# Optimization experiments

Measured on AMD Instinct MI355X. Metric: run time of the kernel, lower is better.

## Reference

```python
import jax, jax.numpy as jnp
import numpy as np


def setup_inputs() -> dict:
    key = jax.random.key(0)
    ks = jax.random.split(key, 9)
    B, L, Dh, Din = 8, 2048, 256, 1024  # Dh = hidden_size = input_dim // num_heads
    s = 0.05
    return {
        "x": jax.random.normal(ks[0], (B, L, Dh), dtype=jnp.float32),
        "Wq": jax.random.normal(ks[1], (Dh, Dh), dtype=jnp.float32) * s,
        "bq": jax.random.normal(ks[2], (Dh,), dtype=jnp.float32) * s,
        "Wk": jax.random.normal(ks[3], (Dh, Dh), dtype=jnp.float32) * s,
        "bk": jax.random.normal(ks[4], (Dh,), dtype=jnp.float32) * s,
        "Wv": jax.random.normal(ks[5], (Dh, Dh), dtype=jnp.float32) * s,
        "bv": jax.random.normal(ks[6], (Dh,), dtype=jnp.float32) * s,
        "Wo": jax.random.normal(ks[7], (Dh, Din), dtype=jnp.float32) * s,
        "bo": jax.random.normal(ks[8], (Din,), dtype=jnp.float32) * s,
        "num_heads": 4,
    }


def reference(x, Wq, bq, Wk, bk, Wv, bv, Wo, bo, num_heads):
    B, L, d = x.shape  # d == hidden_size; scale uses this full dim per the source
    H = num_heads
    hd = d // H
    # QKV projections (weights stored [in, out])
    Q = (x @ Wq + bq).reshape(B, L, H, hd).transpose(0, 2, 1, 3)  # [B,H,L,hd]
    K = (x @ Wk + bk).reshape(B, L, H, hd).transpose(0, 2, 1, 3)
    V = (x @ Wv + bv).reshape(B, L, H, hd).transpose(0, 2, 1, 3)
    scale = 1.0 / jnp.sqrt(jnp.float32(d))  # source divides by dim**0.5 with dim = x.shape[-1]
    scores = jnp.einsum("bhqd,bhkd->bhqk", Q, K) * scale  # [B,H,L,L]
    weights = jax.nn.softmax(scores, axis=-1)
    # dropout is identity in eval mode
    ctx = jnp.einsum("bhqk,bhkd->bhqd", weights, V)  # [B,H,L,hd]
    ctx = ctx.transpose(0, 2, 1, 3).reshape(B, L, d)
    return ctx @ Wo + bo  # [B,L,input_dim]
```

## Files before the change

kernel.cpp:

```cpp
#include <hip/hip_runtime.h>

#define SEQ   2048
#define NH    4
#define HD    64
#define DH    256
#define DIN   1024
#define MTOK  16384
#define BH    32

typedef _Float16 half8 __attribute__((ext_vector_type(8)));
typedef _Float16 half4 __attribute__((ext_vector_type(4)));
typedef float    floatx4 __attribute__((ext_vector_type(4)));

__device__ __forceinline__ floatx4 mfma16(half8 a, half8 b, floatx4 c) {
    return __builtin_amdgcn_mfma_f32_16x16x32_f16(a, b, c, 0, 0, 0);
}

#if __has_builtin(__builtin_amdgcn_exp2f)
#define EXP2(x) __builtin_amdgcn_exp2f(x)
#else
#define EXP2(x) exp2f(x)
#endif

__device__ __forceinline__ int swz(int r, int g) {
    return r * 64 + ((g ^ (r & 7)) << 3);
}

__device__ __forceinline__ void glds16(const _Float16* g, _Float16* l) {
    __builtin_amdgcn_global_load_lds(
        (const __attribute__((address_space(1))) void*)g,
        (__attribute__((address_space(3))) void*)l, 16, 0, 0);
}

#define QSCALE 0.09016844005556021f

__global__ __launch_bounds__(256) void cvt_kernel(
    const float* __restrict__ x, const float* __restrict__ Wq,
    const float* __restrict__ Wk, const float* __restrict__ Wv,
    const float* __restrict__ Wo, _Float16* __restrict__ xh,
    _Float16* __restrict__ Wt)
{
    const int t = threadIdx.x;
    if (blockIdx.x < 2048) {
        const size_t i = ((size_t)blockIdx.x * 256 + t) * 8;
        const float4 f0 = *(const float4*)(x + i);
        const float4 f1 = *(const float4*)(x + i + 4);
        half8 h;
        h[0]=(_Float16)f0.x; h[1]=(_Float16)f0.y; h[2]=(_Float16)f0.z; h[3]=(_Float16)f0.w;
        h[4]=(_Float16)f1.x; h[5]=(_Float16)f1.y; h[6]=(_Float16)f1.z; h[7]=(_Float16)f1.w;
        *(half8*)(xh + i) = h;
        return;
    }
    const int wb = blockIdx.x - 2048;
    const int nb = (wb % 28) * 64;
    const int kb = (wb / 28) * 64;
    const float* src; int ld, nc0;
    if (nb < 768) {
        src = (nb < 256) ? Wq : (nb < 512) ? Wk : Wv;
        ld = DH; nc0 = nb & 255;
    } else { src = Wo; ld = DIN; nc0 = nb - 768; }

    __shared__ float Ts[64][65];
    const int c = t & 63, r0 = t >> 6;
#pragma unroll
    for (int rr = 0; rr < 16; rr++)
        Ts[r0 + rr * 4][c] = src[(size_t)(kb + r0 + rr * 4) * ld + nc0 + c];
    __syncthreads();
    const int nr = t >> 2, kc = (t & 3) * 16;
    _Float16 hv[16];
#pragma unroll
    for (int j = 0; j < 16; j++) hv[j] = (_Float16)Ts[kc + j][nr];
    *(half8*)&Wt[(size_t)(nb + nr) * 256 + kb + kc]     = *(half8*)&hv[0];
    *(half8*)&Wt[(size_t)(nb + nr) * 256 + kb + kc + 8] = *(half8*)&hv[8];
}

__global__ __launch_bounds__(256) void qkv_kernel(
    const _Float16* __restrict__ xh, const _Float16* __restrict__ Wt,
    const float* __restrict__ bq, const float* __restrict__ bk,
    const float* __restrict__ bv,
    _Float16* __restrict__ Qo, _Float16* __restrict__ Ko, _Float16* __restrict__ Vt)
{
    const int mb = blockIdx.x * 128;
    const int nb = blockIdx.y * 128;
    const int t = threadIdx.x, lane = t & 63, w = t >> 6;
    const int quad = lane >> 4, l16 = lane & 15;
    const int wr = (w >> 1) * 64, wc = (w & 1) * 64;

    __shared__ _Float16 Ah[128 * 64];
    __shared__ _Float16 Bh[128 * 64];

    floatx4 acc[4][4] = {};

    const int srow = w * 8 + (lane >> 3);
    const int slg  = (lane & 7) ^ ((lane >> 3) & 7);
    const int sbase = w * 64;

    for (int k0 = 0; k0 < DH; k0 += 64) {
        __syncthreads();
#pragma unroll
        for (int c = 0; c < 4; c++) {
            glds16(xh + (size_t)(mb + c * 32 + srow) * DH + k0 + slg * 8,
                   &Ah[(c * 256 + sbase) * 8]);
            glds16(Wt + (size_t)(nb + c * 32 + srow) * DH + k0 + slg * 8,
                   &Bh[(c * 256 + sbase) * 8]);
        }
        __syncthreads();
#pragma unroll
        for (int kh = 0; kh < 2; kh++) {
            half8 af[4], bf[4];
#pragma unroll
            for (int i = 0; i < 4; i++) {
                af[i] = *(const half8*)&Ah[swz(wr + i * 16 + l16, kh * 4 + quad)];
                bf[i] = *(const half8*)&Bh[swz(wc + i * 16 + l16, kh * 4 + quad)];
            }
#pragma unroll
            for (int mt = 0; mt < 4; mt++)
#pragma unroll
                for (int nt = 0; nt < 4; nt++)
                    acc[mt][nt] = mfma16(af[mt], bf[nt], acc[mt][nt]);
        }
    }

    const int which = nb >> 8;
    const float* bias = (which == 0) ? bq : (which == 1) ? bk : bv;
    const float qs = (which == 0) ? QSCALE : 1.0f;

#pragma unroll
    for (int nt = 0; nt < 4; nt++) {
        const int col = nb + wc + nt * 16 + l16;
        const int c2 = col & 255;
        const float bb = bias[c2];
        const int h = c2 >> 6, hd = c2 & 63;
#pragma unroll
        for (int mt = 0; mt < 4; mt++) {
            const int mr0 = mb + wr + mt * 16 + quad * 4;
            const int b = mr0 >> 11, lt0 = mr0 & (SEQ - 1);
            const int bh = b * NH + h;
            if (which == 2) {
                half4 hv;
#pragma unroll
                for (int i = 0; i < 4; i++) hv[i] = (_Float16)(acc[mt][nt][i] + bb);
                *(half4*)&Vt[((size_t)bh * HD + hd) * SEQ + lt0] = hv;
            } else {
                _Float16* dst = ((which == 0) ? Qo : Ko) + ((size_t)bh * SEQ + lt0) * HD + hd;
#pragma unroll
                for (int i = 0; i < 4; i++)
                    dst[(size_t)i * HD] = (_Float16)((acc[mt][nt][i] + bb) * qs);
            }
        }
    }
}

__global__ __launch_bounds__(256, 4) void attn_kernel(
    const _Float16* __restrict__ Q, const _Float16* __restrict__ K,
    const _Float16* __restrict__ Vt, _Float16* __restrict__ Opart,
    float* __restrict__ Lsum, int kspan)
{
    const int bh = blockIdx.y, qb = blockIdx.x * 128, ks = blockIdx.z;
    const int t = threadIdx.x, lane = t & 63, w = t >> 6;
    const int quad = lane >> 4, l16 = lane & 15;

    __shared__ _Float16 Ksm[64 * 64];
    __shared__ _Float16 Vsm[64 * 64];
    __shared__ _Float16 Psm[4 * 32 * 64];

    const _Float16* Kbh = K + (size_t)bh * SEQ * HD;
    const _Float16* Vbh = Vt + (size_t)bh * HD * SEQ;

    half8 qf[2][2];
#pragma unroll
    for (int qt = 0; qt < 2; qt++) {
        const _Float16* qp = Q + ((size_t)bh * SEQ + qb + w * 32 + qt * 16 + l16) * HD;
        qf[qt][0] = *(const half8*)(qp + quad * 8);
        qf[qt][1] = *(const half8*)(qp + 32 + quad * 8);
    }

    floatx4 oacc[2][4] = {};
    float lsum[2] = {0.f, 0.f};

    const int srow = w * 8 + (lane >> 3);
    const int slg  = (lane & 7) ^ ((lane >> 3) & 7);
    const int sbase = w * 64;
    const int pbase = w * 2048;
    const int kb0 = ks * kspan, kb1 = kb0 + kspan;

    for (int kb = kb0; kb < kb1; kb += 64) {
        __syncthreads();
#pragma unroll
        for (int c = 0; c < 2; c++) {
            glds16(Kbh + (size_t)(kb + c * 32 + srow) * HD + slg * 8,
                   &Ksm[(c * 256 + sbase) * 8]);
            glds16(Vbh + (size_t)(c * 32 + srow) * SEQ + kb + slg * 8,
                   &Vsm[(c * 256 + sbase) * 8]);
        }
        __syncthreads();

#pragma unroll
        for (int kt = 0; kt < 4; kt++) {
            const half8 kf0 = *(const half8*)&Ksm[swz(kt * 16 + l16, quad)];
            const half8 kf1 = *(const half8*)&Ksm[swz(kt * 16 + l16, 4 + quad)];
#pragma unroll
            for (int qt = 0; qt < 2; qt++) {
                floatx4 a = {};
                a = mfma16(kf0, qf[qt][0], a);
                a = mfma16(kf1, qf[qt][1], a);
                const float p0 = EXP2(a[0]), p1 = EXP2(a[1]);
                const float p2 = EXP2(a[2]), p3 = EXP2(a[3]);
                lsum[qt] += (p0 + p1) + (p2 + p3);
                half4 hp;
                hp[0] = (_Float16)p0; hp[1] = (_Float16)p1;
                hp[2] = (_Float16)p2; hp[3] = (_Float16)p3;
                const int g = kt * 2 + (quad >> 1);
                *(half4*)&Psm[pbase + (qt * 16 + l16) * 64 +
                              ((g ^ (l16 & 7)) << 3) + (quad & 1) * 4] = hp;
            }
        }

#pragma unroll
        for (int k2 = 0; k2 < 2; k2++) {
            half8 pf[2];
#pragma unroll
            for (int qt = 0; qt < 2; qt++)
                pf[qt] = *(const half8*)&Psm[pbase + swz(qt * 16 + l16, k2 * 4 + quad)];
#pragma unroll
            for (int nt = 0; nt < 4; nt++) {
                const half8 vf = *(const half8*)&Vsm[swz(nt * 16 + l16, k2 * 4 + quad)];
#pragma unroll
                for (int qt = 0; qt < 2; qt++)
                    oacc[qt][nt] = mfma16(pf[qt], vf, oacc[qt][nt]);
            }
        }
    }

#pragma unroll
    for (int qt = 0; qt < 2; qt++) {
        lsum[qt] += __shfl_xor(lsum[qt], 16, 64);
        lsum[qt] += __shfl_xor(lsum[qt], 32, 64);
        if (quad == 0)
            Lsum[((size_t)(ks * BH + bh)) * SEQ + qb + w * 32 + qt * 16 + l16] = lsum[qt];
    }
    _Float16* op = Opart + (((size_t)(ks * BH + bh)) * SEQ + qb + w * 32) * HD;
#pragma unroll
    for (int qt = 0; qt < 2; qt++)
#pragma unroll
        for (int i = 0; i < 4; i++) {
            const int r = qt * 16 + quad * 4 + i;
#pragma unroll
            for (int nt = 0; nt < 4; nt++)
                op[(size_t)r * HD + nt * 16 + l16] = (_Float16)oacc[qt][nt][i];
        }
}

__global__ __launch_bounds__(256) void reduce_kernel(
    const _Float16* __restrict__ Opart, const float* __restrict__ Lsum,
    _Float16* __restrict__ ctx, int nks)
{
    const size_t i = ((size_t)blockIdx.x * 256 + threadIdx.x) * 8;
    const int ch = (int)(i & 255);
    const int h = ch >> 6, hd = ch & 63;
    const int tok = (int)(i >> 8);
    const int b = tok >> 11, l = tok & (SEQ - 1);
    const int bh = b * NH + h;

    float a[8] = {};
    float lt = 0.f;
    for (int ks = 0; ks < nks; ks++) {
        const size_t row = ((size_t)(ks * BH + bh)) * SEQ + l;
        lt += Lsum[row];
        const half8 v = *(const half8*)(Opart + row * HD + hd);
#pragma unroll
        for (int j = 0; j < 8; j++) a[j] += (float)v[j];
    }
    const float inv = 1.0f / lt;
    half8 o;
#pragma unroll
    for (int j = 0; j < 8; j++) o[j] = (_Float16)(a[j] * inv);
    *(half8*)(ctx + i) = o;
}

__global__ __launch_bounds__(256) void out_kernel(
    const _Float16* __restrict__ ctx, const _Float16* __restrict__ Wot,
    const float* __restrict__ bo, float* __restrict__ out)
{
    const int mb = blockIdx.x * 128;
    const int nb = blockIdx.y * 128;
    const int t = threadIdx.x, lane = t & 63, w = t >> 6;
    const int quad = lane >> 4, l16 = lane & 15;
    const int wr = (w >> 1) * 64, wc = (w & 1) * 64;

    __shared__ _Float16 Ah[128 * 64];
    __shared__ _Float16 Bh[128 * 64];

    floatx4 acc[4][4] = {};

    const int srow = w * 8 + (lane >> 3);
    const int slg  = (lane & 7) ^ ((lane >> 3) & 7);
    const int sbase = w * 64;

    for (int k0 = 0; k0 < DH; k0 += 64) {
        __syncthreads();
#pragma unroll
        for (int c = 0; c < 4; c++) {
            glds16(ctx + (size_t)(mb + c * 32 + srow) * DH + k0 + slg * 8,
                   &Ah[(c * 256 + sbase) * 8]);
            glds16(Wot + (size_t)(nb + c * 32 + srow) * DH + k0 + slg * 8,
                   &Bh[(c * 256 + sbase) * 8]);
        }
        __syncthreads();
#pragma unroll
        for (int kh = 0; kh < 2; kh++) {
            half8 af[4], bf[4];
#pragma unroll
            for (int i = 0; i < 4; i++) {
                af[i] = *(const half8*)&Ah[swz(wr + i * 16 + l16, kh * 4 + quad)];
                bf[i] = *(const half8*)&Bh[swz(wc + i * 16 + l16, kh * 4 + quad)];
            }
#pragma unroll
            for (int mt = 0; mt < 4; mt++)
#pragma unroll
                for (int nt = 0; nt < 4; nt++)
                    acc[mt][nt] = mfma16(af[mt], bf[nt], acc[mt][nt]);
        }
    }

#pragma unroll
    for (int nt = 0; nt < 4; nt++) {
        const int col = nb + wc + nt * 16 + l16;
        const float bb = bo[col];
#pragma unroll
        for (int mt = 0; mt < 4; mt++) {
            const int mr0 = mb + wr + mt * 16 + quad * 4;
            float* dst = out + (size_t)mr0 * DIN + col;
#pragma unroll
            for (int i = 0; i < 4; i++)
                dst[(size_t)i * DIN] = acc[mt][nt][i] + bb;
        }
    }
}

extern "C" void kernel_launch(void* const* d_in, const int* in_sizes, int n_in,
                              void* d_out, int out_size, void* d_ws, size_t ws_size,
                              hipStream_t stream) {
    (void)in_sizes; (void)n_in; (void)out_size;
    const float* x  = (const float*)d_in[0];
    const float* Wq = (const float*)d_in[1];
    const float* bq = (const float*)d_in[2];
    const float* Wk = (const float*)d_in[3];
    const float* bk = (const float*)d_in[4];
    const float* Wv = (const float*)d_in[5];
    const float* bv = (const float*)d_in[6];
    const float* Wo = (const float*)d_in[7];
    const float* bo = (const float*)d_in[8];

    const size_t H = (size_t)BH * SEQ * HD;
    _Float16* Qw = (_Float16*)d_ws;
    _Float16* Kw = Qw + H;
    _Float16* Vt = Kw + H;
    _Float16* xh = Vt + H;
    _Float16* Wt = xh + (size_t)MTOK * DH;
    _Float16* Opart = Wt + (size_t)1792 * 256;

    const size_t need2 = ((size_t)(Opart - Qw) + 2 * H) * 2 + (size_t)2 * BH * SEQ * 4;
    const int KS = (ws_size >= need2) ? 2 : 1;
    float* Lsum = (float*)(Opart + (size_t)KS * H);
    _Float16* Cw = xh;

    cvt_kernel<<<dim3(2048 + 112), 256, 0, stream>>>(x, Wq, Wk, Wv, Wo, xh, Wt);
    qkv_kernel<<<dim3(MTOK / 128, 768 / 128), 256, 0, stream>>>(
        xh, Wt, bq, bk, bv, Qw, Kw, Vt);
    attn_kernel<<<dim3(SEQ / 128, BH, KS), 256, 0, stream>>>(
        Qw, Kw, Vt, Opart, Lsum, SEQ / KS);
    reduce_kernel<<<dim3(MTOK * DH / (256 * 8)), 256, 0, stream>>>(
        Opart, Lsum, Cw, KS);
    out_kernel<<<dim3(MTOK / 128, DIN / 128), 256, 0, stream>>>(
        Cw, Wt + (size_t)768 * DH, bo, (float*)d_out);
}
```

Measured before the change: 171.3 us.

## Fuse split-K reduce into output GEMM, enlarge attention query tile, vectorize stores

Removes the separate reduce kernel by having the output projection GEMM sum the split-K attention partials and apply the softmax normalisation while staging its A tile in shared memory. The attention kernel now handles 256 queries per block (64 per wave) to reuse each K/V tile across more queries, with launch bounds lowered from 4 to 3. MFMA operands are swapped in the QKV, attention and output kernels so results come out transposed, which lets the epilogues write half4/float4 vectors instead of scattered scalars. The trade-offs are higher register and LDS pressure in attention, and redundant partial-sum reads in the output GEMM, since every column block rereads Opart.

```diff
diff --git a/kernel.cpp b/kernel.cpp
--- a/kernel.cpp
+++ b/kernel.cpp
@@ -85,6 +85,7 @@
     const int t = threadIdx.x, lane = t & 63, w = t >> 6;
     const int quad = lane >> 4, l16 = lane & 15;
     const int wr = (w >> 1) * 64, wc = (w & 1) * 64;
+    const int which = nb >> 8;
 
     __shared__ _Float16 Ah[128 * 64];
     __shared__ _Float16 Bh[128 * 64];
@@ -113,75 +114,95 @@
                 af[i] = *(const half8*)&Ah[swz(wr + i * 16 + l16, kh * 4 + quad)];
                 bf[i] = *(const half8*)&Bh[swz(wc + i * 16 + l16, kh * 4 + quad)];
             }
-#pragma unroll
-            for (int mt = 0; mt < 4; mt++)
-#pragma unroll
-                for (int nt = 0; nt < 4; nt++)
-                    acc[mt][nt] = mfma16(af[mt], bf[nt], acc[mt][nt]);
-        }
-    }
-
-    const int which = nb >> 8;
-    const float* bias = (which == 0) ? bq : (which == 1) ? bk : bv;
-    const float qs = (which == 0) ? QSCALE : 1.0f;
-
-#pragma unroll
-    for (int nt = 0; nt < 4; nt++) {
-        const int col = nb + wc + nt * 16 + l16;
-        const int c2 = col & 255;
-        const float bb = bias[c2];
-        const int h = c2 >> 6, hd = c2 & 63;
-#pragma unroll
-        for (int mt = 0; mt < 4; mt++) {
-            const int mr0 = mb + wr + mt * 16 + quad * 4;
-            const int b = mr0 >> 11, lt0 = mr0 & (SEQ - 1);
-            const int bh = b * NH + h;
             if (which == 2) {
+#pragma unroll
+                for (int mt = 0; mt < 4; mt++)
+#pragma unroll
+                    for (int nt = 0; nt < 4; nt++)
+                        acc[mt][nt] = mfma16(af[mt], bf[nt], acc[mt][nt]);
+            } else {
+#pragma unroll
+                for (int mt = 0; mt < 4; mt++)
+#pragma unroll
+                    for (int nt = 0; nt < 4; nt++)
+                        acc[mt][nt] = mfma16(bf[nt], af[mt], acc[mt][nt]);
+            }
+        }
+    }
+
+    if (which == 2) {
+#pragma unroll
+        for (int nt = 0; nt < 4; nt++) {
+            const int c2 = (nb & 255) + wc + nt * 16 + l16;
+            const float bb = bv[c2];
+            const int h = c2 >> 6, hd = c2 & 63;
+#pragma unroll
+            for (int mt = 0; mt < 4; mt++) {
+                const int mr0 = mb + wr + mt * 16 + quad * 4;
+                const int b = mr0 >> 11, lt0 = mr0 & (SEQ - 1);
+                const int bh = b * NH + h;
                 half4 hv;
 #pragma unroll
                 for (int i = 0; i < 4; i++) hv[i] = (_Float16)(acc[mt][nt][i] + bb);
                 *(half4*)&Vt[((size_t)bh * HD + hd) * SEQ + lt0] = hv;
-            } else {
-                _Float16* dst = ((which == 0) ? Qo : Ko) + ((size_t)bh * SEQ + lt0) * HD + hd;
-#pragma unroll
-                for (int i = 0; i < 4; i++)
-                    dst[(size_t)i * HD] = (_Float16)((acc[mt][nt][i] + bb) * qs);
-            }
-        }
-    }
-}
-
-__global__ __launch_bounds__(256, 4) void attn_kernel(
+            }
+        }
+    } else {
+        const float* bias = (which == 0) ? bq : bk;
+        const float qs = (which == 0) ? QSCALE : 1.0f;
+        _Float16* Out = (which == 0) ? Qo : Ko;
+#pragma unroll
+        for (int nt = 0; nt < 4; nt++) {
+            const int c2b = (nb & 255) + wc + nt * 16 + quad * 4;
+            const float4 bb4 = *(const float4*)&bias[c2b];
+            const int h = c2b >> 6, hd0 = c2b & 63;
+#pragma unroll
+            for (int mt = 0; mt < 4; mt++) {
+                const int tok = mb + wr + mt * 16 + l16;
+                const int b = tok >> 11, lt = tok & (SEQ - 1);
+                const int bh = b * NH + h;
+                half4 hv;
+                hv[0] = (_Float16)((acc[mt][nt][0] + bb4.x) * qs);
+                hv[1] = (_Float16)((acc[mt][nt][1] + bb4.y) * qs);
+                hv[2] = (_Float16)((acc[mt][nt][2] + bb4.z) * qs);
+                hv[3] = (_Float16)((acc[mt][nt][3] + bb4.w) * qs);
+                *(half4*)&Out[((size_t)bh * SEQ + lt) * HD + hd0] = hv;
+            }
+        }
+    }
+}
+
+__global__ __launch_bounds__(256, 3) void attn_kernel(
     const _Float16* __restrict__ Q, const _Float16* __restrict__ K,
     const _Float16* __restrict__ Vt, _Float16* __restrict__ Opart,
     float* __restrict__ Lsum, int kspan)
 {
-    const int bh = blockIdx.y, qb = blockIdx.x * 128, ks = blockIdx.z;
+    const int bh = blockIdx.y, qb = blockIdx.x * 256, ks = blockIdx.z;
     const int t = threadIdx.x, lane = t & 63, w = t >> 6;
     const int quad = lane >> 4, l16 = lane & 15;
 
     __shared__ _Float16 Ksm[64 * 64];
     __shared__ _Float16 Vsm[64 * 64];
-    __shared__ _Float16 Psm[4 * 32 * 64];
+    __shared__ _Float16 Psm[4 * 64 * 64];
 
     const _Float16* Kbh = K + (size_t)bh * SEQ * HD;
     const _Float16* Vbh = Vt + (size_t)bh * HD * SEQ;
 
-    half8 qf[2][2];
-#pragma unroll
-    for (int qt = 0; qt < 2; qt++) {
-        const _Float16* qp = Q + ((size_t)bh * SEQ + qb + w * 32 + qt * 16 + l16) * HD;
+    half8 qf[4][2];
+#pragma unroll
+    for (int qt = 0; qt < 4; qt++) {
+        const _Float16* qp = Q + ((size_t)bh * SEQ + qb + w * 64 + qt * 16 + l16) * HD;
         qf[qt][0] = *(const half8*)(qp + quad * 8);
         qf[qt][1] = *(const half8*)(qp + 32 + quad * 8);
     }
 
-    floatx4 oacc[2][4] = {};
-    float lsum[2] = {0.f, 0.f};
+    floatx4 oacc[4][4] = {};
+    float lsum[4] = {};
 
     const int srow = w * 8 + (lane >> 3);
     const int slg  = (lane & 7) ^ ((lane >> 3) & 7);
     const int sbase = w * 64;
-    const int pbase = w * 2048;
+    const int pbase = w * 4096;
     const int kb0 = ks * kspan, kb1 = kb0 + kspan;
 
     for (int kb = kb0; kb < kb1; kb += 64) {
@@ -200,7 +221,7 @@
             const half8 kf0 = *(const half8*)&Ksm[swz(kt * 16 + l16, quad)];
             const half8 kf1 = *(const half8*)&Ksm[swz(kt * 16 + l16, 4 + quad)];
 #pragma unroll
-            for (int qt = 0; qt < 2; qt++) {
+            for (int qt = 0; qt < 4; qt++) {
                 floatx4 a = {};
                 a = mfma16(kf0, qf[qt][0], a);
                 a = mfma16(kf1, qf[qt][1], a);
@@ -218,69 +239,43 @@
 
 #pragma unroll
         for (int k2 = 0; k2 < 2; k2++) {
-            half8 pf[2];
-#pragma unroll
-            for (int qt = 0; qt < 2; qt++)
+            half8 pf[4];
+#pragma unroll
+            for (int qt = 0; qt < 4; qt++)
                 pf[qt] = *(const half8*)&Psm[pbase + swz(qt * 16 + l16, k2 * 4 + quad)];
 #pragma unroll
             for (int nt = 0; nt < 4; nt++) {
                 const half8 vf = *(const half8*)&Vsm[swz(nt * 16 + l16, k2 * 4 + quad)];
 #pragma unroll
-                for (int qt = 0; qt < 2; qt++)
-                    oacc[qt][nt] = mfma16(pf[qt], vf, oacc[qt][nt]);
-            }
-        }
-    }
-
-#pragma unroll
-    for (int qt = 0; qt < 2; qt++) {
+                for (int qt = 0; qt < 4; qt++)
+                    oacc[qt][nt] = mfma16(vf, pf[qt], oacc[qt][nt]);
+            }
+        }
+    }
+
+#pragma unroll
+    for (int qt = 0; qt < 4; qt++) {
         lsum[qt] += __shfl_xor(lsum[qt], 16, 64);
         lsum[qt] += __shfl_xor(lsum[qt], 32, 64);
         if (quad == 0)
-            Lsum[((size_t)(ks * BH + bh)) * SEQ + qb + w * 32 + qt * 16 + l16] = lsum[qt];
-    }
-    _Float16* op = Opart + (((size_t)(ks * BH + bh)) * SEQ + qb + w * 32) * HD;
-#pragma unroll
-    for (int qt = 0; qt < 2; qt++)
-#pragma unroll
-        for (int i = 0; i < 4; i++) {
-            const int r = qt * 16 + quad * 4 + i;
-#pragma unroll
-            for (int nt = 0; nt < 4; nt++)
-                op[(size_t)r * HD + nt * 16 + l16] = (_Float16)oacc[qt][nt][i];
-        }
-}
-
-__global__ __launch_bounds__(256) void reduce_kernel(
+            Lsum[((size_t)(ks * BH + bh)) * SEQ + qb + w * 64 + qt * 16 + l16] = lsum[qt];
+    }
+    _Float16* op = Opart + (((size_t)(ks * BH + bh)) * SEQ + qb + w * 64) * HD;
+#pragma unroll
+    for (int qt = 0; qt < 4; qt++)
+#pragma unroll
+        for (int nt = 0; nt < 4; nt++) {
+            half4 hv;
+#pragma unroll
+            for (int i = 0; i < 4; i++) hv[i] = (_Float16)oacc[qt][nt][i];
+            *(half4*)&op[(size_t)(qt * 16 + l16) * HD + nt * 16 + quad * 4] = hv;
+        }
+}
+
+__global__ __launch_bounds__(256) void out_kernel(
     const _Float16* __restrict__ Opart, const float* __restrict__ Lsum,
-    _Float16* __restrict__ ctx, int nks)
-{
-    const size_t i = ((size_t)blockIdx.x * 256 + threadIdx.x) * 8;
-    const int ch = (int)(i & 255);
-    const int h = ch >> 6, hd = ch & 63;
-    const int tok = (int)(i >> 8);
-    const int b = tok >> 11, l = tok & (SEQ - 1);
-    const int bh = b * NH + h;
-
-    float a[8] = {};
-    float lt = 0.f;
-    for (int ks = 0; ks < nks; ks++) {
-        const size_t row = ((size_t)(ks * BH + bh)) * SEQ + l;
-        lt += Lsum[row];
-        const half8 v = *(const half8*)(Opart + row * HD + hd);
-#pragma unroll
-        for (int j = 0; j < 8; j++) a[j] += (float)v[j];
-    }
-    const float inv = 1.0f / lt;
-    half8 o;
-#pragma unroll
-    for (int j = 0; j < 8; j++) o[j] = (_Float16)(a[j] * inv);
-    *(half8*)(ctx + i) = o;
-}
-
-__global__ __launch_bounds__(256) void out_kernel(
-    const _Float16* __restrict__ ctx, const _Float16* __restrict__ Wot,
-    const float* __restrict__ bo, float* __restrict__ out)
+    const _Float16* __restrict__ Wot, const float* __restrict__ bo,
+    float* __restrict__ out, int nks)
 {
     const int mb = blockIdx.x * 128;
     const int nb = blockIdx.y * 128;
@@ -296,15 +291,34 @@
     const int srow = w * 8 + (lane >> 3);
     const int slg  = (lane & 7) ^ ((lane >> 3) & 7);
     const int sbase = w * 64;
+    const int ar  = t >> 1;
+    const int ag0 = (t & 1) * 4;
+    const int b   = mb >> 11;
+    const int tok_l = (mb & (SEQ - 1)) + ar;
 
     for (int k0 = 0; k0 < DH; k0 += 64) {
         __syncthreads();
-#pragma unroll
-        for (int c = 0; c < 4; c++) {
-            glds16(ctx + (size_t)(mb + c * 32 + srow) * DH + k0 + slg * 8,
-                   &Ah[(c * 256 + sbase) * 8]);
+        const int bhh = b * NH + (k0 >> 6);
+#pragma unroll
+        for (int c = 0; c < 4; c++)
             glds16(Wot + (size_t)(nb + c * 32 + srow) * DH + k0 + slg * 8,
                    &Bh[(c * 256 + sbase) * 8]);
+        {
+            float lt = 0.f;
+            for (int k2 = 0; k2 < nks; k2++)
+                lt += Lsum[((size_t)(k2 * BH + bhh)) * SEQ + tok_l];
+            const _Float16 invh = (_Float16)(1.0f / lt);
+#pragma unroll
+            for (int u = 0; u < 4; u++) {
+                const int g = ag0 + u;
+                half8 s = {};
+                for (int k2 = 0; k2 < nks; k2++)
+                    s += *(const half8*)(Opart +
+                        (((size_t)(k2 * BH + bhh)) * SEQ + tok_l) * HD + g * 8);
+#pragma unroll
+                for (int j = 0; j < 8; j++) s[j] *= invh;
+                *(half8*)&Ah[ar * 64 + ((g ^ (ar & 7)) << 3)] = s;
+            }
         }
         __syncthreads();
 #pragma unroll
@@ -319,21 +333,23 @@
             for (int mt = 0; mt < 4; mt++)
 #pragma unroll
                 for (int nt = 0; nt < 4; nt++)
-                    acc[mt][nt] = mfma16(af[mt], bf[nt], acc[mt][nt]);
+                    acc[mt][nt] = mfma16(bf[nt], af[mt], acc[mt][nt]);
         }
     }
 
 #pragma unroll
     for (int nt = 0; nt < 4; nt++) {
-        const int col = nb + wc + nt * 16 + l16;
-        const float bb = bo[col];
+        const int col0 = nb + wc + nt * 16 + quad * 4;
+        const float4 bb4 = *(const float4*)&bo[col0];
 #pragma unroll
         for (int mt = 0; mt < 4; mt++) {
-            const int mr0 = mb + wr + mt * 16 + quad * 4;
-            float* dst = out + (size_t)mr0 * DIN + col;
-#pragma unroll
-            for (int i = 0; i < 4; i++)
-                dst[(size_t)i * DIN] = acc[mt][nt][i] + bb;
+            const int tok = mb + wr + mt * 16 + l16;
+            float4 ov;
+            ov.x = acc[mt][nt][0] + bb4.x;
+            ov.y = acc[mt][nt][1] + bb4.y;
+            ov.z = acc[mt][nt][2] + bb4.z;
+            ov.w = acc[mt][nt][3] + bb4.w;
+            *(float4*)&out[(size_t)tok * DIN + col0] = ov;
         }
     }
 }
@@ -360,18 +376,16 @@
     _Float16* Wt = xh + (size_t)MTOK * DH;
     _Float16* Opart = Wt + (size_t)1792 * 256;
 
-    const size_t need2 = ((size_t)(Opart - Qw) + 2 * H) * 2 + (size_t)2 * BH * SEQ * 4;
-    const int KS = (ws_size >= need2) ? 2 : 1;
+    const size_t base_bytes = (3 * H + (size_t)MTOK * DH + (size_t)1792 * 256) * 2;
+    const size_t per_ks = H * 2 + (size_t)BH * SEQ * 4;
+    const int KS = (ws_size >= base_bytes + 2 * per_ks) ? 2 : 1;
     float* Lsum = (float*)(Opart + (size_t)KS * H);
-    _Float16* Cw = xh;
 
     cvt_kernel<<<dim3(2048 + 112), 256, 0, stream>>>(x, Wq, Wk, Wv, Wo, xh, Wt);
     qkv_kernel<<<dim3(MTOK / 128, 768 / 128), 256, 0, stream>>>(
         xh, Wt, bq, bk, bv, Qw, Kw, Vt);
-    attn_kernel<<<dim3(SEQ / 128, BH, KS), 256, 0, stream>>>(
+    attn_kernel<<<dim3(SEQ / 256, BH, KS), 256, 0, stream>>>(
         Qw, Kw, Vt, Opart, Lsum, SEQ / KS);
-    reduce_kernel<<<dim3(MTOK * DH / (256 * 8)), 256, 0, stream>>>(
-        Opart, Lsum, Cw, KS);
     out_kernel<<<dim3(MTOK / 128, DIN / 128), 256, 0, stream>>>(
-        Cw, Wt + (size_t)768 * DH, bo, (float*)d_out);
-}
+        Opart, Lsum, Wt + (size_t)768 * DH, bo, (float*)d_out, KS);
+}
```

New measurement: 212.9 us. 1.24x slower.

## Swap MFMA operands for vectorized epilogue stores and raise key-split count

Applied to the files above, without the earlier changes.

Swaps the A/B operands of the MFMA in the Q/K projection, the attention PV product and the output GEMM so each lane holds four consecutive columns, then writes outputs with half4/float4 vector stores instead of strided scalar stores. It also reorganises the workspace so Opart can overlap the converted inputs and the context buffer reuses the Q region. The attention key split goes from 2 to 4 when the workspace is large enough. This reduces the number of store instructions and uncoalesced writes, and adds attention parallelism, at the cost of more partial-result traffic for the reduce kernel and tighter buffer-aliasing assumptions.

```diff
diff --git a/kernel.cpp b/kernel.cpp
--- a/kernel.cpp
+++ b/kernel.cpp
@@ -38,7 +38,7 @@
     const float* __restrict__ x, const float* __restrict__ Wq,
     const float* __restrict__ Wk, const float* __restrict__ Wv,
     const float* __restrict__ Wo, _Float16* __restrict__ xh,
-    _Float16* __restrict__ Wt)
+    _Float16* __restrict__ Wtq, _Float16* __restrict__ WoT)
 {
     const int t = threadIdx.x;
     if (blockIdx.x < 2048) {
@@ -55,10 +55,11 @@
     const int nb = (wb % 28) * 64;
     const int kb = (wb / 28) * 64;
     const float* src; int ld, nc0;
+    _Float16* dstbase; int nrow0;
     if (nb < 768) {
         src = (nb < 256) ? Wq : (nb < 512) ? Wk : Wv;
-        ld = DH; nc0 = nb & 255;
-    } else { src = Wo; ld = DIN; nc0 = nb - 768; }
+        ld = DH; nc0 = nb & 255; dstbase = Wtq; nrow0 = nb;
+    } else { src = Wo; ld = DIN; nc0 = nb - 768; dstbase = WoT; nrow0 = nb - 768; }
 
     __shared__ float Ts[64][65];
     const int c = t & 63, r0 = t >> 6;
@@ -70,12 +71,12 @@
     _Float16 hv[16];
 #pragma unroll
     for (int j = 0; j < 16; j++) hv[j] = (_Float16)Ts[kc + j][nr];
-    *(half8*)&Wt[(size_t)(nb + nr) * 256 + kb + kc]     = *(half8*)&hv[0];
-    *(half8*)&Wt[(size_t)(nb + nr) * 256 + kb + kc + 8] = *(half8*)&hv[8];
+    *(half8*)&dstbase[(size_t)(nrow0 + nr) * 256 + kb + kc]     = *(half8*)&hv[0];
+    *(half8*)&dstbase[(size_t)(nrow0 + nr) * 256 + kb + kc + 8] = *(half8*)&hv[8];
 }
 
 __global__ __launch_bounds__(256) void qkv_kernel(
-    const _Float16* __restrict__ xh, const _Float16* __restrict__ Wt,
+    const _Float16* __restrict__ xh, const _Float16* __restrict__ Wtq,
     const float* __restrict__ bq, const float* __restrict__ bk,
     const float* __restrict__ bv,
     _Float16* __restrict__ Qo, _Float16* __restrict__ Ko, _Float16* __restrict__ Vt)
@@ -85,6 +86,7 @@
     const int t = threadIdx.x, lane = t & 63, w = t >> 6;
     const int quad = lane >> 4, l16 = lane & 15;
     const int wr = (w >> 1) * 64, wc = (w & 1) * 64;
+    const int which = nb >> 8;
 
     __shared__ _Float16 Ah[128 * 64];
     __shared__ _Float16 Bh[128 * 64];
@@ -101,7 +103,7 @@
         for (int c = 0; c < 4; c++) {
             glds16(xh + (size_t)(mb + c * 32 + srow) * DH + k0 + slg * 8,
                    &Ah[(c * 256 + sbase) * 8]);
-            glds16(Wt + (size_t)(nb + c * 32 + srow) * DH + k0 + slg * 8,
+            glds16(Wtq + (size_t)(nb + c * 32 + srow) * DH + k0 + slg * 8,
                    &Bh[(c * 256 + sbase) * 8]);
         }
         __syncthreads();
@@ -113,39 +115,59 @@
                 af[i] = *(const half8*)&Ah[swz(wr + i * 16 + l16, kh * 4 + quad)];
                 bf[i] = *(const half8*)&Bh[swz(wc + i * 16 + l16, kh * 4 + quad)];
             }
-#pragma unroll
-            for (int mt = 0; mt < 4; mt++)
-#pragma unroll
-                for (int nt = 0; nt < 4; nt++)
-                    acc[mt][nt] = mfma16(af[mt], bf[nt], acc[mt][nt]);
-        }
-    }
-
-    const int which = nb >> 8;
-    const float* bias = (which == 0) ? bq : (which == 1) ? bk : bv;
-    const float qs = (which == 0) ? QSCALE : 1.0f;
-
-#pragma unroll
-    for (int nt = 0; nt < 4; nt++) {
-        const int col = nb + wc + nt * 16 + l16;
-        const int c2 = col & 255;
-        const float bb = bias[c2];
-        const int h = c2 >> 6, hd = c2 & 63;
-#pragma unroll
-        for (int mt = 0; mt < 4; mt++) {
-            const int mr0 = mb + wr + mt * 16 + quad * 4;
-            const int b = mr0 >> 11, lt0 = mr0 & (SEQ - 1);
-            const int bh = b * NH + h;
             if (which == 2) {
+#pragma unroll
+                for (int mt = 0; mt < 4; mt++)
+#pragma unroll
+                    for (int nt = 0; nt < 4; nt++)
+                        acc[mt][nt] = mfma16(af[mt], bf[nt], acc[mt][nt]);
+            } else {
+#pragma unroll
+                for (int mt = 0; mt < 4; mt++)
+#pragma unroll
+                    for (int nt = 0; nt < 4; nt++)
+                        acc[mt][nt] = mfma16(bf[nt], af[mt], acc[mt][nt]);
+            }
+        }
+    }
+
+    if (which == 2) {
+#pragma unroll
+        for (int nt = 0; nt < 4; nt++) {
+            const int c2 = (nb & 255) + wc + nt * 16 + l16;
+            const float bb = bv[c2];
+            const int h = c2 >> 6, hd = c2 & 63;
+#pragma unroll
+            for (int mt = 0; mt < 4; mt++) {
+                const int mr0 = mb + wr + mt * 16 + quad * 4;
+                const int b = mr0 >> 11, lt0 = mr0 & (SEQ - 1);
+                const int bh = b * NH + h;
                 half4 hv;
 #pragma unroll
                 for (int i = 0; i < 4; i++) hv[i] = (_Float16)(acc[mt][nt][i] + bb);
                 *(half4*)&Vt[((size_t)bh * HD + hd) * SEQ + lt0] = hv;
-            } else {
-                _Float16* dst = ((which == 0) ? Qo : Ko) + ((size_t)bh * SEQ + lt0) * HD + hd;
-#pragma unroll
-                for (int i = 0; i < 4; i++)
-                    dst[(size_t)i * HD] = (_Float16)((acc[mt][nt][i] + bb) * qs);
+            }
+        }
+    } else {
+        const float* bias = (which == 0) ? bq : bk;
+        const float qs = (which == 0) ? QSCALE : 1.0f;
+        _Float16* Out = (which == 0) ? Qo : Ko;
+#pragma unroll
+        for (int nt = 0; nt < 4; nt++) {
+            const int c2b = (nb & 255) + wc + nt * 16 + quad * 4;
+            const float4 bb4 = *(const float4*)&bias[c2b];
+            const int h = c2b >> 6, hd0 = c2b & 63;
+#pragma unroll
+            for (int mt = 0; mt < 4; mt++) {
+                const int tok = mb + wr + mt * 16 + l16;
+                const int b = tok >> 11, lt = tok & (SEQ - 1);
+                const int bh = b * NH + h;
+                half4 hv;
+                hv[0] = (_Float16)((acc[mt][nt][0] + bb4.x) * qs);
+                hv[1] = (_Float16)((acc[mt][nt][1] + bb4.y) * qs);
+                hv[2] = (_Float16)((acc[mt][nt][2] + bb4.z) * qs);
+                hv[3] = (_Float16)((acc[mt][nt][3] + bb4.w) * qs);
+                *(half4*)&Out[((size_t)bh * SEQ + lt) * HD + hd0] = hv;
             }
         }
     }
@@ -227,7 +249,7 @@
                 const half8 vf = *(const half8*)&Vsm[swz(nt * 16 + l16, k2 * 4 + quad)];
 #pragma unroll
                 for (int qt = 0; qt < 2; qt++)
-                    oacc[qt][nt] = mfma16(pf[qt], vf, oacc[qt][nt]);
+                    oacc[qt][nt] = mfma16(vf, pf[qt], oacc[qt][nt]);
             }
         }
     }
@@ -243,11 +265,11 @@
 #pragma unroll
     for (int qt = 0; qt < 2; qt++)
 #pragma unroll
-        for (int i = 0; i < 4; i++) {
-            const int r = qt * 16 + quad * 4 + i;
-#pragma unroll
-            for (int nt = 0; nt < 4; nt++)
-                op[(size_t)r * HD + nt * 16 + l16] = (_Float16)oacc[qt][nt][i];
+        for (int nt = 0; nt < 4; nt++) {
+            half4 hv;
+#pragma unroll
+            for (int i = 0; i < 4; i++) hv[i] = (_Float16)oacc[qt][nt][i];
+            *(half4*)&op[(size_t)(qt * 16 + l16) * HD + nt * 16 + quad * 4] = hv;
         }
 }
 
@@ -279,7 +301,7 @@
 }
 
 __global__ __launch_bounds__(256) void out_kernel(
-    const _Float16* __restrict__ ctx, const _Float16* __restrict__ Wot,
+    const _Float16* __restrict__ ctx, const _Float16* __restrict__ WoT,
     const float* __restrict__ bo, float* __restrict__ out)
 {
     const int mb = blockIdx.x * 128;
@@ -303,7 +325,7 @@
         for (int c = 0; c < 4; c++) {
             glds16(ctx + (size_t)(mb + c * 32 + srow) * DH + k0 + slg * 8,
                    &Ah[(c * 256 + sbase) * 8]);
-            glds16(Wot + (size_t)(nb + c * 32 + srow) * DH + k0 + slg * 8,
+            glds16(WoT + (size_t)(nb + c * 32 + srow) * DH + k0 + slg * 8,
                    &Bh[(c * 256 + sbase) * 8]);
         }
         __syncthreads();
@@ -319,21 +341,23 @@
             for (int mt = 0; mt < 4; mt++)
 #pragma unroll
                 for (int nt = 0; nt < 4; nt++)
-                    acc[mt][nt] = mfma16(af[mt], bf[nt], acc[mt][nt]);
+                    acc[mt][nt] = mfma16(bf[nt], af[mt], acc[mt][nt]);
         }
     }
 
 #pragma unroll
     for (int nt = 0; nt < 4; nt++) {
-        const int col = nb + wc + nt * 16 + l16;
-        const float bb = bo[col];
+        const int col0 = nb + wc + nt * 16 + quad * 4;
+        const float4 bb4 = *(const float4*)&bo[col0];
 #pragma unroll
         for (int mt = 0; mt < 4; mt++) {
-            const int mr0 = mb + wr + mt * 16 + quad * 4;
-            float* dst = out + (size_t)mr0 * DIN + col;
-#pragma unroll
-            for (int i = 0; i < 4; i++)
-                dst[(size_t)i * DIN] = acc[mt][nt][i] + bb;
+            const int tok = mb + wr + mt * 16 + l16;
+            float4 ov;
+            ov.x = acc[mt][nt][0] + bb4.x;
+            ov.y = acc[mt][nt][1] + bb4.y;
+            ov.z = acc[mt][nt][2] + bb4.z;
+            ov.w = acc[mt][nt][3] + bb4.w;
+            *(float4*)&out[(size_t)tok * DIN + col0] = ov;
         }
     }
 }
@@ -353,25 +377,28 @@
     const float* bo = (const float*)d_in[8];
 
     const size_t H = (size_t)BH * SEQ * HD;
-    _Float16* Qw = (_Float16*)d_ws;
-    _Float16* Kw = Qw + H;
-    _Float16* Vt = Kw + H;
-    _Float16* xh = Vt + H;
-    _Float16* Wt = xh + (size_t)MTOK * DH;
-    _Float16* Opart = Wt + (size_t)1792 * 256;
-
-    const size_t need2 = ((size_t)(Opart - Qw) + 2 * H) * 2 + (size_t)2 * BH * SEQ * 4;
-    const int KS = (ws_size >= need2) ? 2 : 1;
-    float* Lsum = (float*)(Opart + (size_t)KS * H);
-    _Float16* Cw = xh;
-
-    cvt_kernel<<<dim3(2048 + 112), 256, 0, stream>>>(x, Wq, Wk, Wv, Wo, xh, Wt);
+    _Float16* Qw  = (_Float16*)d_ws;
+    _Float16* Kw  = Qw + H;
+    _Float16* Vt  = Kw + H;
+    _Float16* WoT = Vt + H;
+    const size_t lsum_off = 3 * H + 262144;
+
+    const size_t need4 = lsum_off * 2 + (size_t)4 * 65536 * 4 + (size_t)4 * H * 2;
+    const int KS = (ws_size >= need4) ? 4 : 2;
+
+    float* Lsum = (float*)(Qw + lsum_off);
+    _Float16* Opart = Qw + lsum_off + (size_t)KS * 131072;
+    _Float16* xh  = Opart;
+    _Float16* Wtq = Opart + (size_t)MTOK * DH;
+    _Float16* ctx = Qw;
+
+    cvt_kernel<<<dim3(2048 + 112), 256, 0, stream>>>(x, Wq, Wk, Wv, Wo, xh, Wtq, WoT);
     qkv_kernel<<<dim3(MTOK / 128, 768 / 128), 256, 0, stream>>>(
-        xh, Wt, bq, bk, bv, Qw, Kw, Vt);
+        xh, Wtq, bq, bk, bv, Qw, Kw, Vt);
     attn_kernel<<<dim3(SEQ / 128, BH, KS), 256, 0, stream>>>(
         Qw, Kw, Vt, Opart, Lsum, SEQ / KS);
     reduce_kernel<<<dim3(MTOK * DH / (256 * 8)), 256, 0, stream>>>(
-        Opart, Lsum, Cw, KS);
+        Opart, Lsum, ctx, KS);
     out_kernel<<<dim3(MTOK / 128, DIN / 128), 256, 0, stream>>>(
-        Cw, Wt + (size_t)768 * DH, bo, (float*)d_out);
-}
+        ctx, WoT, bo, (float*)d_out);
+}
```

New measurement: 194.7 us. 1.14x slower.
